# Performance work log

Hardware: AMD Instinct MI355X
Metric: run time of the kernel (lower is better)

Reference implementation:

```python
import jax, jax.numpy as jnp
import numpy as np

B, T, D = 4, 4096, 1024
EPS = 1e-5


def _layernorm(x, w):
    mu = jnp.mean(x, axis=-1, keepdims=True)
    var = jnp.var(x, axis=-1, keepdims=True)
    return (x - mu) * jax.lax.rsqrt(var + EPS) * w


def setup_inputs() -> dict:
    key = jax.random.key(0)
    k0, k1, k2, k3 = jax.random.split(key, 4)
    x = jax.random.normal(k0, (B, T, D), dtype=jnp.float32)
    lengths = jax.random.randint(k1, (B,), 1, T + 1, dtype=jnp.int32)
    ln1_w = jnp.ones((D,), dtype=jnp.float32)
    ln2_w = jnp.ones((D,), dtype=jnp.float32)
    Wfc = jax.random.normal(k2, (D, 4 * D), dtype=jnp.float32) * 0.02
    Wproj = jax.random.normal(k3, (4 * D, D), dtype=jnp.float32) * 0.02
    return {"x": x, "lengths": lengths, "ln1_w": ln1_w, "ln2_w": ln2_w,
            "Wfc": Wfc, "Wproj": Wproj}


def reference(x, lengths, ln1_w, ln2_w, Wfc, Wproj):
    b, t, d = x.shape
    # valid[b, i] = i < lengths[b]  (non-padded positions)
    valid = (jnp.arange(t)[None, :] < lengths[:, None]).astype(x.dtype)  # (B,T)

    # --- FusedQueryAtt: out[b,i] = h[b,i] + valid_i * sum_{j<=i} valid_j * gelu(h[b,j])
    h = _layernorm(x, ln1_w)
    g = jax.nn.gelu(h, approximate=False) * valid[:, :, None]  # (B,T,D)
    attn_out = h + valid[:, :, None] * jnp.cumsum(g, axis=1)
    x = x + attn_out  # residual around attn

    # --- MLP (bias=False, dropout=0 in eval)
    h2 = _layernorm(x, ln2_w)
    mlp_out = jax.nn.gelu(h2 @ Wfc, approximate=False) @ Wproj
    return x + mlp_out
```

## Files before the change

kernel.cpp:

```cpp
#include <hip/hip_runtime.h>
#include <hip/hip_bf16.h>
#include <math.h>

#define B_SZ 4
#define T_SZ 4096
#define D_SZ 1024
#define H_SZ 4096
#define CHUNK 16
#define NCHUNK (T_SZ / CHUNK)
#define LN_EPS 1e-5f

using frag8 = __attribute__((ext_vector_type(8))) short;
using f32x4 = __attribute__((ext_vector_type(4))) float;

__device__ __forceinline__ float gelu_exact(float x) {
  return 0.5f * x * (1.0f + erff(x * 0.70710678118654752f));
}

__device__ __forceinline__ float gelu_fast(float x) {
  float u2 = 1.5957691216057308f * (x + 0.044715f * x * x * x);
  float e = __expf(u2);
  return x - x * __builtin_amdgcn_rcpf(e + 1.0f);
}

__device__ __forceinline__ unsigned short f2bf(float f) {
  unsigned u = __float_as_uint(f);
  u += 0x7fffu + ((u >> 16) & 1u);
  return (unsigned short)(u >> 16);
}

__global__ __launch_bounds__(256) void ln_stats(
    const float* __restrict__ x, float2* __restrict__ stats) {
  __shared__ float red[8];
  int tid = threadIdx.x;
  size_t row = (size_t)blockIdx.x * D_SZ;
  float4 v = ((const float4*)(x + row))[tid];
  float s = v.x + v.y + v.z + v.w;
  float q = v.x * v.x + v.y * v.y + v.z * v.z + v.w * v.w;
#pragma unroll
  for (int o = 32; o > 0; o >>= 1) {
    s += __shfl_xor(s, o, 64);
    q += __shfl_xor(q, o, 64);
  }
  int w = tid >> 6;
  if ((tid & 63) == 0) { red[w * 2] = s; red[w * 2 + 1] = q; }
  __syncthreads();
  if (tid == 0) {
    s = red[0] + red[2] + red[4] + red[6];
    q = red[1] + red[3] + red[5] + red[7];
    float mu = s * (1.0f / D_SZ);
    float var = q * (1.0f / D_SZ) - mu * mu;
    float2 st; st.x = mu; st.y = rsqrtf(var + LN_EPS);
    stats[blockIdx.x] = st;
  }
}

__global__ __launch_bounds__(256) void attn_phase1(
    const float* __restrict__ x, const float2* __restrict__ stats,
    const int* __restrict__ lengths, const float* __restrict__ w1,
    float* __restrict__ partial, float* __restrict__ csum) {
  int b = blockIdx.x >> 8;
  int c = blockIdx.x & (NCHUNK - 1);
  int tid = threadIdx.x;
  int len = lengths[b];
  float4 w = ((const float4*)w1)[tid];
  float run0 = 0.f, run1 = 0.f, run2 = 0.f, run3 = 0.f;
#pragma unroll 4
  for (int i = 0; i < CHUNK; ++i) {
    int t = c * CHUNK + i;
    size_t row = ((size_t)b * T_SZ + t) * D_SZ;
    float4 v = ((const float4*)(x + row))[tid];
    float2 st = stats[b * T_SZ + t];
    bool valid = t < len;
    float hx = (v.x - st.x) * st.y * w.x, hy = (v.y - st.x) * st.y * w.y;
    float hz = (v.z - st.x) * st.y * w.z, hw = (v.w - st.x) * st.y * w.w;
    if (valid) {
      run0 += gelu_exact(hx); run1 += gelu_exact(hy);
      run2 += gelu_exact(hz); run3 += gelu_exact(hw);
    }
    float4 p;
    p.x = v.x + hx + (valid ? run0 : 0.f);
    p.y = v.y + hy + (valid ? run1 : 0.f);
    p.z = v.z + hz + (valid ? run2 : 0.f);
    p.w = v.w + hw + (valid ? run3 : 0.f);
    ((float4*)(partial + row))[tid] = p;
  }
  float4 cs; cs.x = run0; cs.y = run1; cs.z = run2; cs.w = run3;
  ((float4*)(csum + ((size_t)b * NCHUNK + c) * D_SZ))[tid] = cs;
}

__global__ __launch_bounds__(256) void chunk_scan(float* __restrict__ csum) {
  int idx = blockIdx.x * 256 + threadIdx.x;
  int b = idx >> 10;
  int d = idx & (D_SZ - 1);
  float* p = csum + (size_t)b * NCHUNK * D_SZ + d;
  float acc = 0.f;
#pragma unroll 8
  for (int c = 0; c < NCHUNK; ++c) {
    float t = p[(size_t)c * D_SZ];
    p[(size_t)c * D_SZ] = acc;
    acc += t;
  }
}

__global__ __launch_bounds__(256) void attn_phase2_ln2(
    float* __restrict__ xres, const float* __restrict__ csum,
    const int* __restrict__ lengths, const float* __restrict__ w2,
    unsigned short* __restrict__ h2) {
  __shared__ float red[8];
  int t = blockIdx.x & (T_SZ - 1);
  int b = blockIdx.x >> 12;
  int tid = threadIdx.x;
  bool valid = t < lengths[b];
  int c = t / CHUNK;
  size_t row = ((size_t)b * T_SZ + t) * D_SZ;
  float4 v = ((const float4*)(xres + row))[tid];
  if (valid) {
    float4 o = ((const float4*)(csum + ((size_t)b * NCHUNK + c) * D_SZ))[tid];
    v.x += o.x; v.y += o.y; v.z += o.z; v.w += o.w;
  }
  ((float4*)(xres + row))[tid] = v;
  float s = v.x + v.y + v.z + v.w;
  float q = v.x * v.x + v.y * v.y + v.z * v.z + v.w * v.w;
#pragma unroll
  for (int o = 32; o > 0; o >>= 1) {
    s += __shfl_xor(s, o, 64);
    q += __shfl_xor(q, o, 64);
  }
  int wv = tid >> 6;
  if ((tid & 63) == 0) { red[wv * 2] = s; red[wv * 2 + 1] = q; }
  __syncthreads();
  s = red[0] + red[2] + red[4] + red[6];
  q = red[1] + red[3] + red[5] + red[7];
  float mu = s * (1.0f / D_SZ);
  float var = q * (1.0f / D_SZ) - mu * mu;
  float rstd = rsqrtf(var + LN_EPS);
  float4 w = ((const float4*)w2)[tid];
  ushort4 hq;
  hq.x = f2bf((v.x - mu) * rstd * w.x);
  hq.y = f2bf((v.y - mu) * rstd * w.y);
  hq.z = f2bf((v.z - mu) * rstd * w.z);
  hq.w = f2bf((v.w - mu) * rstd * w.w);
  ((ushort4*)(h2 + row))[tid] = hq;
}

__global__ __launch_bounds__(256) void transpose_f32_to_bf16(
    const float* __restrict__ src, unsigned short* __restrict__ dst,
    int R, int C) {
  __shared__ float tile[32][33];
  int bx = blockIdx.x * 32;
  int by = blockIdx.y * 32;
  int tx = threadIdx.x & 31;
  int ty = threadIdx.x >> 5;
#pragma unroll
  for (int i = 0; i < 32; i += 8)
    tile[ty + i][tx] = src[(size_t)(by + ty + i) * C + bx + tx];
  __syncthreads();
#pragma unroll
  for (int i = 0; i < 32; i += 8)
    dst[(size_t)(bx + ty + i) * R + by + tx] = f2bf(tile[tx][ty + i]);
}

__device__ __forceinline__ void gld_lds16(const unsigned short* g,
                                          unsigned short* l) {
  __builtin_amdgcn_global_load_lds(
      (const __attribute__((address_space(1))) unsigned int*)g,
      (__attribute__((address_space(3))) unsigned int*)l, 16, 0, 0);
}

#define GT_TILE (256 * 64)

__device__ __forceinline__ void stageA(const unsigned short* A_blk, int K,
                                       unsigned short* as_buf, int h, int k0,
                                       int tid) {
#pragma unroll
  for (int j = 0; j < 2; ++j) {
    int R = j * 128 + h * 64 + (tid >> 3);
    int kc = ((tid & 7) * 8) ^ ((R & 7) << 3);
    gld_lds16(A_blk + (size_t)R * K + k0 + kc,
              as_buf + R * 64 + (tid & 7) * 8);
  }
}

__device__ __forceinline__ void stageB(const unsigned short* B_blk, int K,
                                       unsigned short* bs_buf, int h, int k0,
                                       int tid) {
  int lr = tid >> 3;
#pragma unroll
  for (int j = 0; j < 2; ++j) {
    int R = j * 128 + (lr >> 5) * 64 + h * 32 + (lr & 31);
    int kc = ((tid & 7) * 8) ^ ((R & 7) << 3);
    gld_lds16(B_blk + (size_t)R * K + k0 + kc,
              bs_buf + R * 64 + (tid & 7) * 8);
  }
}

__device__ __forceinline__ void load_afrag(const unsigned short* base,
                                           frag8 (&dst)[4][2], int mh, int wm,
                                           int r16, int quad) {
#pragma unroll
  for (int tm = 0; tm < 4; ++tm)
#pragma unroll
    for (int kk = 0; kk < 2; ++kk) {
      int r = wm * 128 + mh * 64 + tm * 16 + r16;
      int cb = (kk * 64 + quad * 16) ^ ((r16 & 7) << 4);
      dst[tm][kk] = *(const frag8*)(base + r * 64 + (cb >> 1));
    }
}

__device__ __forceinline__ void load_bfrag(const unsigned short* base,
                                           frag8 (&dst)[2][2], int nh, int wn,
                                           int r16, int quad) {
#pragma unroll
  for (int tn = 0; tn < 2; ++tn)
#pragma unroll
    for (int kk = 0; kk < 2; ++kk) {
      int r = wn * 64 + nh * 32 + tn * 16 + r16;
      int cb = (kk * 64 + quad * 16) ^ ((r16 & 7) << 4);
      dst[tn][kk] = *(const frag8*)(base + r * 64 + (cb >> 1));
    }
}

template <int MH, int NH>
__device__ __forceinline__ void mfma_q(f32x4 (&acc)[8][4],
                                       const frag8 (&a)[4][2],
                                       const frag8 (&b)[2][2]) {
#pragma unroll
  for (int kk = 0; kk < 2; ++kk)
#pragma unroll
    for (int tm = 0; tm < 4; ++tm)
#pragma unroll
      for (int tn = 0; tn < 2; ++tn)
        acc[MH * 4 + tm][NH * 2 + tn] =
            __builtin_amdgcn_mfma_f32_16x16x32_bf16(
                a[tm][kk], b[tn][kk], acc[MH * 4 + tm][NH * 2 + tn], 0, 0, 0);
}

#define GBAR()                          \
  do {                                  \
    asm volatile("" ::: "memory");      \
    __builtin_amdgcn_s_barrier();       \
    asm volatile("" ::: "memory");      \
  } while (0)

__global__ __launch_bounds__(512, 2) void gemm256_bt(
    const unsigned short* __restrict__ A, const unsigned short* __restrict__ Bt,
    int N, int K, int gx,
    const float* __restrict__ resid, float* __restrict__ outf,
    unsigned short* __restrict__ outb, int epi) {
  extern __shared__ unsigned short smem[];
  unsigned short* As = smem;
  unsigned short* Bs = smem + 2 * GT_TILE;

  int orig = blockIdx.x, nwg = gridDim.x;
  int wg = orig;
  if ((nwg & 7) == 0) wg = (orig & 7) * (nwg >> 3) + (orig >> 3);
  int bx = wg % gx, by = wg / gx;
  int bm = by * 256, bn = bx * 256;

  int tid = threadIdx.x;
  int lane = tid & 63, wave = tid >> 6;
  int wm = wave >> 2, wn = wave & 3;
  int quad = lane >> 4, r16 = lane & 15;

  const unsigned short* A_blk = A + (size_t)bm * K;
  const unsigned short* B_blk = Bt + (size_t)bn * K;
  int nt = K >> 6;

  f32x4 acc[8][4] = {};
  frag8 af[4][2];
  frag8 b0[2][2], b1[2][2];

  stageA(A_blk, K, As, 0, 0, tid);
  stageA(A_blk, K, As, 1, 0, tid);
  stageB(B_blk, K, Bs, 0, 0, tid);
  stageB(B_blk, K, Bs, 1, 0, tid);
  if (nt > 1) {
    stageA(A_blk, K, As + GT_TILE, 0, 64, tid);
    stageB(B_blk, K, Bs + GT_TILE, 0, 64, tid);
    stageB(B_blk, K, Bs + GT_TILE, 1, 64, tid);
    asm volatile("s_waitcnt vmcnt(6)" ::: "memory");
  } else {
    asm volatile("s_waitcnt vmcnt(0)" ::: "memory");
  }
  GBAR();
  load_bfrag(Bs, b0, 0, wn, r16, quad);

  for (int t = 0; t < nt; ++t) {
    unsigned short* As_c = As + (t & 1) * GT_TILE;
    unsigned short* Bs_c = Bs + (t & 1) * GT_TILE;
    unsigned short* As_n = As + ((t + 1) & 1) * GT_TILE;
    unsigned short* Bs_n = Bs + ((t + 1) & 1) * GT_TILE;
    bool p1 = (t + 1 < nt), p2 = (t + 2 < nt);

    load_afrag(As_c, af, 0, wm, r16, quad);
    if (p1) stageA(A_blk, K, As_n, 1, (t + 1) * 64, tid);
    GBAR();
    __builtin_amdgcn_s_setprio(1);
    mfma_q<0, 0>(acc, af, b0);
    __builtin_amdgcn_s_setprio(0);
    GBAR();

    load_bfrag(Bs_c, b1, 1, wn, r16, quad);
    if (p2) stageA(A_blk, K, As_c, 0, (t + 2) * 64, tid);
    GBAR();
    __builtin_amdgcn_s_setprio(1);
    mfma_q<0, 1>(acc, af, b1);
    __builtin_amdgcn_s_setprio(0);
    GBAR();

    load_afrag(As_c, af, 1, wm, r16, quad);
    if (p2) stageB(B_blk, K, Bs_c, 0, (t + 2) * 64, tid);
    GBAR();
    __builtin_amdgcn_s_setprio(1);
    mfma_q<1, 1>(acc, af, b1);
    __builtin_amdgcn_s_setprio(0);
    GBAR();

    if (p2) {
      stageB(B_blk, K, Bs_c, 1, (t + 2) * 64, tid);
      asm volatile("s_waitcnt vmcnt(6)" ::: "memory");
    } else {
      asm volatile("s_waitcnt vmcnt(0)" ::: "memory");
    }
    GBAR();
    __builtin_amdgcn_s_setprio(1);
    mfma_q<1, 0>(acc, af, b0);
    __builtin_amdgcn_s_setprio(0);
    if (p1) load_bfrag(Bs_n, b0, 0, wn, r16, quad);
    GBAR();
  }

  if (epi == 0) {
#pragma unroll
    for (int mf = 0; mf < 8; ++mf) {
#pragma unroll
      for (int nf = 0; nf < 4; ++nf) {
        int gm0 = bm + wm * 128 + mf * 16 + quad * 4;
        int gn = bn + wn * 64 + nf * 16 + r16;
#pragma unroll
        for (int r = 0; r < 4; ++r)
          outb[(size_t)(gm0 + r) * N + gn] = f2bf(gelu_fast(acc[mf][nf][r]));
      }
    }
  } else {
#pragma unroll
    for (int mf = 0; mf < 8; ++mf) {
#pragma unroll
      for (int nf = 0; nf < 4; ++nf) {
        int gm0 = bm + wm * 128 + mf * 16 + quad * 4;
        int gn = bn + wn * 64 + nf * 16 + r16;
#pragma unroll
        for (int r = 0; r < 4; ++r)
          outf[(size_t)(gm0 + r) * N + gn] =
              resid[(size_t)(gm0 + r) * N + gn] + acc[mf][nf][r];
      }
    }
  }
}

extern "C" void kernel_launch(void* const* d_in, const int* in_sizes, int n_in,
                              void* d_out, int out_size, void* d_ws,
                              size_t ws_size, hipStream_t stream) {
  const float* x = (const float*)d_in[0];
  const int* lengths = (const int*)d_in[1];
  const float* ln1_w = (const float*)d_in[2];
  const float* ln2_w = (const float*)d_in[3];
  const float* Wfc = (const float*)d_in[4];
  const float* Wproj = (const float*)d_in[5];
  float* out = (float*)d_out;

  static bool lds_cfg = false;
  if (!lds_cfg) {
    hipFuncSetAttribute((const void*)gemm256_bt,
                        hipFuncAttributeMaxDynamicSharedMemorySize, 131072);
    lds_cfg = true;
  }

  char* ws = (char*)d_ws;
  size_t off = 0;
  float2* stats = (float2*)(ws + off);
  off += (size_t)B_SZ * T_SZ * sizeof(float2);
  float* csum = (float*)(ws + off);
  off += (size_t)B_SZ * NCHUNK * D_SZ * sizeof(float);
  unsigned short* wfcb = (unsigned short*)(ws + off);
  off += (size_t)D_SZ * H_SZ * sizeof(unsigned short);
  unsigned short* wprojb = (unsigned short*)(ws + off);
  off += (size_t)H_SZ * D_SZ * sizeof(unsigned short);
  unsigned short* h2 = (unsigned short*)(ws + off);
  off += (size_t)B_SZ * T_SZ * D_SZ * sizeof(unsigned short);
  unsigned short* act = (unsigned short*)(ws + off);

  const int M = B_SZ * T_SZ;
  const size_t tileBytes = 256ull * H_SZ * sizeof(unsigned short);
  size_t avail = (ws_size > off) ? (ws_size - off) : 0;
  int sliceTiles = (int)(avail / tileBytes);
  if (sliceTiles < 1) sliceTiles = 1;
  int sliceM = sliceTiles * 256;
  if (sliceM > M) sliceM = M;

  ln_stats<<<B_SZ * T_SZ, 256, 0, stream>>>(x, stats);
  attn_phase1<<<B_SZ * NCHUNK, 256, 0, stream>>>(x, stats, lengths, ln1_w,
                                                 out, csum);
  chunk_scan<<<(B_SZ * D_SZ) / 256, 256, 0, stream>>>(csum);
  attn_phase2_ln2<<<B_SZ * T_SZ, 256, 0, stream>>>(out, csum, lengths, ln2_w, h2);
  transpose_f32_to_bf16<<<dim3(H_SZ / 32, D_SZ / 32), 256, 0, stream>>>(
      Wfc, wfcb, D_SZ, H_SZ);
  transpose_f32_to_bf16<<<dim3(D_SZ / 32, H_SZ / 32), 256, 0, stream>>>(
      Wproj, wprojb, H_SZ, D_SZ);

  for (int m0 = 0; m0 < M; m0 += sliceM) {
    int rows = (M - m0 < sliceM) ? (M - m0) : sliceM;
    int r1 = rows / 256;
    gemm256_bt<<<dim3((H_SZ / 256) * r1), 512, 131072, stream>>>(
        h2 + (size_t)m0 * D_SZ, wfcb, H_SZ, D_SZ, H_SZ / 256,
        nullptr, nullptr, act, 0);
    gemm256_bt<<<dim3((D_SZ / 256) * r1), 512, 131072, stream>>>(
        act, wprojb, D_SZ, H_SZ, D_SZ / 256,
        out + (size_t)m0 * D_SZ, out + (size_t)m0 * D_SZ, nullptr, 1);
  }
}
```

Before: 487.6 us.

## Merge GEMM main loop into two phases with interleaved A-fragment LDS reads

Restructures the bf16 GEMM inner loop from four barrier-separated MFMA quarters into two halves. Each half walks the M sub-tiles and reads the next A fragment pair from LDS while the current pair's MFMAs run. Both B halves are kept in registers for the whole step, and the three next-next tile stage loads are issued together. This halves the barriers per K-step and lets LDS reads hide behind MFMAs. The cost is that both B fragment sets stay live, and global loads are issued in a burst rather than spread across phases.

```diff
diff --git a/kernel.cpp b/kernel.cpp
--- a/kernel.cpp
+++ b/kernel.cpp
@@ -195,17 +195,15 @@
   }
 }
 
-__device__ __forceinline__ void load_afrag(const unsigned short* base,
-                                           frag8 (&dst)[4][2], int mh, int wm,
-                                           int r16, int quad) {
-#pragma unroll
-  for (int tm = 0; tm < 4; ++tm)
-#pragma unroll
-    for (int kk = 0; kk < 2; ++kk) {
-      int r = wm * 128 + mh * 64 + tm * 16 + r16;
-      int cb = (kk * 64 + quad * 16) ^ ((r16 & 7) << 4);
-      dst[tm][kk] = *(const frag8*)(base + r * 64 + (cb >> 1));
-    }
+__device__ __forceinline__ void read_a_pair(const unsigned short* base,
+                                            frag8 (&dst)[2], int mh, int tm,
+                                            int wm, int r16, int quad) {
+#pragma unroll
+  for (int kk = 0; kk < 2; ++kk) {
+    int r = wm * 128 + mh * 64 + tm * 16 + r16;
+    int cb = (kk * 64 + quad * 16) ^ ((r16 & 7) << 4);
+    dst[kk] = *(const frag8*)(base + r * 64 + (cb >> 1));
+  }
 }
 
 __device__ __forceinline__ void load_bfrag(const unsigned short* base,
@@ -221,19 +219,16 @@
     }
 }
 
-template <int MH, int NH>
-__device__ __forceinline__ void mfma_q(f32x4 (&acc)[8][4],
-                                       const frag8 (&a)[4][2],
-                                       const frag8 (&b)[2][2]) {
+__device__ __forceinline__ void mfma_g(f32x4 (&acc)[8][4], const frag8 (&a)[2],
+                                       const frag8 (&b)[2][2], int mh, int tm,
+                                       int nh) {
 #pragma unroll
   for (int kk = 0; kk < 2; ++kk)
 #pragma unroll
-    for (int tm = 0; tm < 4; ++tm)
-#pragma unroll
-      for (int tn = 0; tn < 2; ++tn)
-        acc[MH * 4 + tm][NH * 2 + tn] =
-            __builtin_amdgcn_mfma_f32_16x16x32_bf16(
-                a[tm][kk], b[tn][kk], acc[MH * 4 + tm][NH * 2 + tn], 0, 0, 0);
+    for (int tn = 0; tn < 2; ++tn)
+      acc[mh * 4 + tm][nh * 2 + tn] =
+          __builtin_amdgcn_mfma_f32_16x16x32_bf16(
+              a[kk], b[tn][kk], acc[mh * 4 + tm][nh * 2 + tn], 0, 0, 0);
 }
 
 #define GBAR()                          \
@@ -268,7 +263,7 @@
   int nt = K >> 6;
 
   f32x4 acc[8][4] = {};
-  frag8 af[4][2];
+  frag8 af[2][2];
   frag8 b0[2][2], b1[2][2];
 
   stageA(A_blk, K, As, 0, 0, tid);
@@ -284,7 +279,9 @@
     asm volatile("s_waitcnt vmcnt(0)" ::: "memory");
   }
   GBAR();
+  read_a_pair(As, af[0], 0, 0, wm, r16, quad);
   load_bfrag(Bs, b0, 0, wn, r16, quad);
+  load_bfrag(Bs, b1, 1, wn, r16, quad);
 
   for (int t = 0; t < nt; ++t) {
     unsigned short* As_c = As + (t & 1) * GT_TILE;
@@ -293,31 +290,22 @@
     unsigned short* Bs_n = Bs + ((t + 1) & 1) * GT_TILE;
     bool p1 = (t + 1 < nt), p2 = (t + 2 < nt);
 
-    load_afrag(As_c, af, 0, wm, r16, quad);
     if (p1) stageA(A_blk, K, As_n, 1, (t + 1) * 64, tid);
     GBAR();
     __builtin_amdgcn_s_setprio(1);
-    mfma_q<0, 0>(acc, af, b0);
+#pragma unroll
+    for (int tm = 0; tm < 4; ++tm) {
+      if (tm < 3) read_a_pair(As_c, af[(tm + 1) & 1], 0, tm + 1, wm, r16, quad);
+      mfma_g(acc, af[tm & 1], b0, 0, tm, 0);
+      mfma_g(acc, af[tm & 1], b1, 0, tm, 1);
+    }
     __builtin_amdgcn_s_setprio(0);
     GBAR();
 
-    load_bfrag(Bs_c, b1, 1, wn, r16, quad);
-    if (p2) stageA(A_blk, K, As_c, 0, (t + 2) * 64, tid);
-    GBAR();
-    __builtin_amdgcn_s_setprio(1);
-    mfma_q<0, 1>(acc, af, b1);
-    __builtin_amdgcn_s_setprio(0);
-    GBAR();
-
-    load_afrag(As_c, af, 1, wm, r16, quad);
-    if (p2) stageB(B_blk, K, Bs_c, 0, (t + 2) * 64, tid);
-    GBAR();
-    __builtin_amdgcn_s_setprio(1);
-    mfma_q<1, 1>(acc, af, b1);
-    __builtin_amdgcn_s_setprio(0);
-    GBAR();
-
+    read_a_pair(As_c, af[0], 1, 0, wm, r16, quad);
     if (p2) {
+      stageA(A_blk, K, As_c, 0, (t + 2) * 64, tid);
+      stageB(B_blk, K, Bs_c, 0, (t + 2) * 64, tid);
       stageB(B_blk, K, Bs_c, 1, (t + 2) * 64, tid);
       asm volatile("s_waitcnt vmcnt(6)" ::: "memory");
     } else {
@@ -325,9 +313,18 @@
     }
     GBAR();
     __builtin_amdgcn_s_setprio(1);
-    mfma_q<1, 0>(acc, af, b0);
+#pragma unroll
+    for (int tm = 0; tm < 4; ++tm) {
+      if (tm < 3) read_a_pair(As_c, af[(tm + 1) & 1], 1, tm + 1, wm, r16, quad);
+      mfma_g(acc, af[tm & 1], b1, 1, tm, 1);
+      mfma_g(acc, af[tm & 1], b0, 1, tm, 0);
+    }
     __builtin_amdgcn_s_setprio(0);
-    if (p1) load_bfrag(Bs_n, b0, 0, wn, r16, quad);
+    if (p1) {
+      load_bfrag(Bs_n, b0, 0, wn, r16, quad);
+      load_bfrag(Bs_n, b1, 1, wn, r16, quad);
+      read_a_pair(As_n, af[0], 0, 0, wm, r16, quad);
+    }
     GBAR();
   }
 
```

After: 497.6 us. +2.1%, slower.
